# Performance work log

Hardware: AMD Instinct MI355X
Metric: run time of the kernel (lower is better)

The kernel has to match this reference:

```python
import jax, jax.numpy as jnp
import numpy as np

N, E = 100000, 800000
NODE_DIM, EDGE_DIM, HIDDEN = 64, 32, 128
LN_EPS = 1e-5


def _linear_params(key, fan_in, fan_out):
    # torch nn.Linear default: U(-1/sqrt(fan_in), 1/sqrt(fan_in))
    kw, kb = jax.random.split(key)
    bound = 1.0 / np.sqrt(fan_in)
    W = jax.random.uniform(kw, (fan_in, fan_out), jnp.float32, -bound, bound)
    b = jax.random.uniform(kb, (fan_out,), jnp.float32, -bound, bound)
    return W, b


def setup_inputs() -> dict:
    key = jax.random.key(0)
    ks = jax.random.split(key, 8)
    x = jax.random.normal(ks[0], (N, NODE_DIM), jnp.float32)
    edge_index = jax.random.randint(ks[1], (2, E), 0, N, jnp.int32)
    edge_attr = jax.random.normal(ks[2], (E, EDGE_DIM), jnp.float32)

    msg_in = 2 * NODE_DIM + EDGE_DIM
    W_msg1, b_msg1 = _linear_params(ks[3], msg_in, HIDDEN)
    g_msg = jnp.ones((HIDDEN,), jnp.float32)
    be_msg = jnp.zeros((HIDDEN,), jnp.float32)
    W_msg2, b_msg2 = _linear_params(ks[4], HIDDEN, HIDDEN)

    upd_in = NODE_DIM + HIDDEN
    W_upd1, b_upd1 = _linear_params(ks[5], upd_in, HIDDEN)
    g_upd = jnp.ones((HIDDEN,), jnp.float32)
    be_upd = jnp.zeros((HIDDEN,), jnp.float32)
    W_upd2, b_upd2 = _linear_params(ks[6], HIDDEN, NODE_DIM)

    return {
        "x": x, "edge_index": edge_index, "edge_attr": edge_attr,
        "W_msg1": W_msg1, "b_msg1": b_msg1, "g_msg": g_msg, "be_msg": be_msg,
        "W_msg2": W_msg2, "b_msg2": b_msg2,
        "W_upd1": W_upd1, "b_upd1": b_upd1, "g_upd": g_upd, "be_upd": be_upd,
        "W_upd2": W_upd2, "b_upd2": b_upd2,
    }


def _layer_norm(h, gamma, beta):
    mu = jnp.mean(h, axis=-1, keepdims=True)
    var = jnp.mean(jnp.square(h - mu), axis=-1, keepdims=True)
    return (h - mu) * jax.lax.rsqrt(var + LN_EPS) * gamma + beta


def _mlp(h, W1, b1, gamma, beta, W2, b2):
    h = h @ W1 + b1
    h = jax.nn.silu(_layer_norm(h, gamma, beta))
    return h @ W2 + b2


def reference(x, edge_index, edge_attr,
              W_msg1, b_msg1, g_msg, be_msg, W_msg2, b_msg2,
              W_upd1, b_upd1, g_upd, be_upd, W_upd2, b_upd2):
    src, dst = edge_index[0], edge_index[1]
    # gather -> message MLP: (E, 2*node_dim + edge_dim) -> (E, hidden)
    msg_input = jnp.concatenate([x[src], x[dst], edge_attr], axis=-1)
    msgs = _mlp(msg_input, W_msg1, b_msg1, g_msg, be_msg, W_msg2, b_msg2)
    # scatter-add aggregate over destination nodes: (N, hidden)
    agg = jax.ops.segment_sum(msgs, dst, num_segments=x.shape[0])
    # update MLP + residual: (N, node_dim)
    upd_input = jnp.concatenate([x, agg], axis=-1)
    return x + _mlp(upd_input, W_upd1, b_upd1, g_upd, be_upd, W_upd2, b_upd2)
```

## Files before the change

kernel.cpp:

```cpp
#include <hip/hip_runtime.h>
#include <hip/hip_fp16.h>
#include <stdint.h>


#define N_NODES 100000
#define N_EDGES 800000
#define NODE_DIM 64
#define EDGE_DIM 32
#define HIDDEN 128
#define LN_EPS 1e-5f

#define PH 136
#define PX 72
#define PU 200
#define PE 36

#define NB_SCAN ((N_NODES + 1023) / 1024)

typedef __attribute__((ext_vector_type(8))) short short8;
typedef __attribute__((ext_vector_type(4))) float f32x4;

static __device__ __forceinline__ uint16_t f2bf(float f) {
  uint32_t u = __float_as_uint(f);
  return (uint16_t)((u + 0x7FFFu + ((u >> 16) & 1u)) >> 16);
}
static __device__ __forceinline__ float bflo(uint32_t u) {
  return __uint_as_float(u << 16);
}
static __device__ __forceinline__ float bfhi(uint32_t u) {
  return __uint_as_float(u & 0xFFFF0000u);
}
static __device__ __forceinline__ float bfs(uint16_t u) {
  return __uint_as_float(((uint32_t)u) << 16);
}


#define PREP_HIST_BLKS 3125
#define PREP_PACK_BLKS 209

__global__ void prep_kernel(const int* __restrict__ ei, int* __restrict__ cnt,
                            const float* __restrict__ W1, uint16_t* __restrict__ Wcatp,
                            uint16_t* __restrict__ W1cb,
                            const float* __restrict__ Wu1, uint16_t* __restrict__ Wu1p,
                            const float* __restrict__ Wu2, uint16_t* __restrict__ Wu2p,
                            const float* __restrict__ W2, const float* __restrict__ b2,
                            float* __restrict__ qv) {
  int b = blockIdx.x;
  if (b < PREP_HIST_BLKS) {
    int e = b * 256 + threadIdx.x;
    if (e < N_EDGES) atomicAdd(&cnt[ei[N_EDGES + e]], 1);
    return;
  }
  int i = (b - PREP_HIST_BLKS) * 256 + threadIdx.x;
  if (i < 16384) {
    int k = i >> 8, c = i & 255;
    float v = (c < 128) ? W1[k * 128 + c] : W1[(64 + k) * 128 + (c - 128)];
    Wcatp[(((k >> 5) * 256 + c) * 4 + ((k >> 3) & 3)) * 8 + (k & 7)] = f2bf(v);
  } else if (i < 24576) {
    i -= 16384;
    int k = i >> 7, c = i & 127;
    Wu1p[(((k >> 5) * 128 + c) * 4 + ((k >> 3) & 3)) * 8 + (k & 7)] = f2bf(Wu1[i]);
  } else if (i < 32768) {
    i -= 24576;
    int k = i >> 6, c = i & 63;
    Wu2p[(((k >> 5) * 64 + c) * 4 + ((k >> 3) & 3)) * 8 + (k & 7)] = f2bf(Wu2[i]);
  } else if (i < 36864) {
    i -= 32768;
    int k = i >> 7, c = i & 127;
    W1cb[((size_t)(c * 4) + ((k >> 3) & 3)) * 8 + (k & 7)] = f2bf(W1[(128 + k) * 128 + c]);
  } else if (i < 53248) {
    i -= 36864;
    int k = i >> 7, c = i & 127;
    float s = 0.f;
    for (int j = 0; j < 128; ++j) s += W2[k * 128 + j] * Wu1[(64 + j) * 128 + c];
    int kk = 64 + k;
    Wu1p[(((kk >> 5) * 128 + c) * 4 + ((kk >> 3) & 3)) * 8 + (kk & 7)] = f2bf(s);
  } else if (i < 53376) {
    int c = i - 53248;
    float s = 0.f;
    for (int j = 0; j < 128; ++j) s += b2[j] * Wu1[(64 + j) * 128 + c];
    qv[c] = s;
  }
}


__global__ __launch_bounds__(256) void scan_blk(const int* __restrict__ cnt,
                                                int* __restrict__ offs,
                                                int* __restrict__ bsum) {
  __shared__ int wsum[4];
  int tid = threadIdx.x;
  int base = blockIdx.x * 1024 + tid * 4;
  int v0 = 0, v1 = 0, v2 = 0, v3 = 0;
  if (base < N_NODES) v0 = cnt[base];
  if (base + 1 < N_NODES) v1 = cnt[base + 1];
  if (base + 2 < N_NODES) v2 = cnt[base + 2];
  if (base + 3 < N_NODES) v3 = cnt[base + 3];
  int tsum = v0 + v1 + v2 + v3;
  int lane = tid & 63, wid = tid >> 6;
  int s = tsum;
  #pragma unroll
  for (int d = 1; d < 64; d <<= 1) {
    int t = __shfl_up(s, d);
    if (lane >= d) s += t;
  }
  if (lane == 63) wsum[wid] = s;
  __syncthreads();
  int woff = 0;
  for (int w = 0; w < wid; ++w) woff += wsum[w];
  int excl = woff + s - tsum;
  if (base < N_NODES) {
    int run = excl;
    offs[base] = run; run += v0;
    if (base + 1 < N_NODES) { offs[base + 1] = run; run += v1; }
    if (base + 2 < N_NODES) { offs[base + 2] = run; run += v2; }
    if (base + 3 < N_NODES) { offs[base + 3] = run; run += v3; }
  }
  if (tid == 255) bsum[blockIdx.x] = woff + s;
}

__global__ void scan_top(int* __restrict__ bsum) {
  __shared__ int sh[128];
  int tid = threadIdx.x;
  int v = (tid < NB_SCAN) ? bsum[tid] : 0;
  int orig = v;
  sh[tid] = v;
  __syncthreads();
  for (int d = 1; d < 128; d <<= 1) {
    int t = (tid >= d) ? sh[tid - d] : 0;
    __syncthreads();
    v += t;
    sh[tid] = v;
    __syncthreads();
  }
  if (tid < NB_SCAN) bsum[tid] = v - orig;
}

__global__ void scan_add(const int* __restrict__ offs, const int* __restrict__ bsum,
                         int* __restrict__ cursor) {
  int i = blockIdx.x * 256 + threadIdx.x;
  if (i < N_NODES) cursor[i] = offs[i] + bsum[i >> 10];
}

__global__ void scatter_edges(const int* __restrict__ ei, int* __restrict__ cursor,
                              int2* __restrict__ se_s, int* __restrict__ dst_s) {
  int e = blockIdx.x * 256 + threadIdx.x;
  if (e < N_EDGES) {
    int s = ei[e], d = ei[N_EDGES + e];
    int p = atomicAdd(&cursor[d], 1);
    se_s[p] = make_int2(s, e);
    dst_s[p] = d;
  }
}


__global__ __launch_bounds__(256) void p12_kernel(
    const float* __restrict__ x, const uint16_t* __restrict__ Wcatp,
    uint16_t* __restrict__ P12) {
  __shared__ __align__(16) uint16_t A[64 * PX];
  const int tid = threadIdx.x;
  const int n0 = blockIdx.x * 64;

  #pragma unroll
  for (int it = 0; it < 4; ++it) {
    int u = tid + it * 256;
    int r = u >> 4, q = u & 15;
    int node = min(n0 + r, N_NODES - 1);
    float4 f = *(const float4*)(x + (size_t)node * 64 + q * 4);
    ushort4 o;
    o.x = f2bf(f.x); o.y = f2bf(f.y); o.z = f2bf(f.z); o.w = f2bf(f.w);
    *(ushort4*)(&A[r * PX + q * 4]) = o;
  }
  __syncthreads();

  const int wid = tid >> 6, lane = tid & 63;
  const int lrow = lane & 15, lk = lane >> 4;
  const int r0 = wid * 16;

  f32x4 acc[16] = {};
  const uint16_t* Abase = &A[(r0 + lrow) * PX + lk * 8];
  #pragma unroll
  for (int c = 0; c < 2; ++c) {
    short8 a = *(const short8*)(Abase + c * 32);
    #pragma unroll
    for (int n = 0; n < 16; ++n) {
      short8 b = *(const short8*)(Wcatp + ((size_t)(c * 256 + n * 16 + lrow) * 4 + lk) * 8);
      acc[n] = __builtin_amdgcn_mfma_f32_16x16x32_bf16(a, b, acc[n], 0, 0, 0);
    }
  }

  #pragma unroll
  for (int reg = 0; reg < 4; ++reg) {
    int row = n0 + r0 + lk * 4 + reg;
    if (row < N_NODES) {
      #pragma unroll
      for (int n = 0; n < 16; ++n) {
        P12[(size_t)row * 256 + n * 16 + lrow] = f2bf(acc[n][reg]);
      }
    }
  }
}


__global__ __launch_bounds__(256) void msg_fused(
    const int2* __restrict__ se_s, const int* __restrict__ dst_s,
    const float* __restrict__ ea,
    const uint16_t* __restrict__ P12, const uint16_t* __restrict__ W1cb,
    const float* __restrict__ b1, const float* __restrict__ g1,
    const float* __restrict__ be1, float* __restrict__ S) {
  __shared__ __align__(16) uint16_t Ae[64 * PE];
  __shared__ __align__(16) uint16_t Hs[64 * PH];
  __shared__ int sdst[64];

  const int tid = threadIdx.x;
  int bid = blockIdx.x;
  int xcd = bid & 7, idx = bid >> 3;
  int bswz = (xcd < 4 ? xcd * 1563 : 6252 + (xcd - 4) * 1562) + idx;
  const int e0 = bswz * 64;

  if (tid < 64) sdst[tid] = dst_s[e0 + tid];

  {
    int pl = tid >> 2, q = tid & 3;
    int eid = se_s[e0 + pl].y;
    const float* er = ea + (size_t)eid * 32 + q * 8;
    float4 f0 = *(const float4*)(er);
    float4 f1 = *(const float4*)(er + 4);
    ushort4 o0, o1;
    o0.x = f2bf(f0.x); o0.y = f2bf(f0.y); o0.z = f2bf(f0.z); o0.w = f2bf(f0.w);
    o1.x = f2bf(f1.x); o1.y = f2bf(f1.y); o1.z = f2bf(f1.z); o1.w = f2bf(f1.w);
    *(ushort4*)(&Ae[pl * PE + q * 8]) = o0;
    *(ushort4*)(&Ae[pl * PE + q * 8 + 4]) = o1;
  }
  __syncthreads();

  const int wid = tid >> 6, lane = tid & 63;
  const int lrow = lane & 15, lk = lane >> 4;
  const int r0 = wid * 16;

  f32x4 acc[8] = {};
  short8 a = *(const short8*)(&Ae[(r0 + lrow) * PE + lk * 8]);
  #pragma unroll
  for (int n = 0; n < 8; ++n) {
    short8 b = *(const short8*)(W1cb + ((size_t)((n * 16 + lrow) * 4) + lk) * 8);
    acc[n] = __builtin_amdgcn_mfma_f32_16x16x32_bf16(a, b, acc[n], 0, 0, 0);
  }
  #pragma unroll
  for (int reg = 0; reg < 4; ++reg) {
    uint16_t* hrow = &Hs[(r0 + lk * 4 + reg) * PH];
    #pragma unroll
    for (int n = 0; n < 8; ++n) {
      hrow[n * 16 + lrow] = f2bf(acc[n][reg]);
    }
  }

  const int g = lk;
  const int c0 = lrow * 8;
  float b1v[8], gv[8], bev[8];
  {
    float4 f0 = *(const float4*)(b1 + c0), f1 = *(const float4*)(b1 + c0 + 4);
    b1v[0]=f0.x; b1v[1]=f0.y; b1v[2]=f0.z; b1v[3]=f0.w;
    b1v[4]=f1.x; b1v[5]=f1.y; b1v[6]=f1.z; b1v[7]=f1.w;
    float4 g0 = *(const float4*)(g1 + c0), g1v = *(const float4*)(g1 + c0 + 4);
    gv[0]=g0.x; gv[1]=g0.y; gv[2]=g0.z; gv[3]=g0.w;
    gv[4]=g1v.x; gv[5]=g1v.y; gv[6]=g1v.z; gv[7]=g1v.w;
    float4 be0 = *(const float4*)(be1 + c0), be1v = *(const float4*)(be1 + c0 + 4);
    bev[0]=be0.x; bev[1]=be0.y; bev[2]=be0.z; bev[3]=be0.w;
    bev[4]=be1v.x; bev[5]=be1v.y; bev[6]=be1v.z; bev[7]=be1v.w;
  }

  #pragma unroll
  for (int it = 0; it < 4; ++it) {
    int er_ = r0 + it * 4 + g;
    int p = e0 + er_;
    int src = se_s[p].x;
    int d = sdst[er_];
    uint4 p1 = *(const uint4*)(P12 + (size_t)src * 256 + c0);
    uint4 p2 = *(const uint4*)(P12 + (size_t)d * 256 + 128 + c0);
    uint4 et = *(const uint4*)(&Hs[er_ * PH + c0]);
    float h[8];
    h[0] = b1v[0] + bflo(p1.x) + bflo(p2.x) + bflo(et.x);
    h[1] = b1v[1] + bfhi(p1.x) + bfhi(p2.x) + bfhi(et.x);
    h[2] = b1v[2] + bflo(p1.y) + bflo(p2.y) + bflo(et.y);
    h[3] = b1v[3] + bfhi(p1.y) + bfhi(p2.y) + bfhi(et.y);
    h[4] = b1v[4] + bflo(p1.z) + bflo(p2.z) + bflo(et.z);
    h[5] = b1v[5] + bfhi(p1.z) + bfhi(p2.z) + bfhi(et.z);
    h[6] = b1v[6] + bflo(p1.w) + bflo(p2.w) + bflo(et.w);
    h[7] = b1v[7] + bfhi(p1.w) + bfhi(p2.w) + bfhi(et.w);

    float s = 0.f, ss = 0.f;
    #pragma unroll
    for (int j = 0; j < 8; ++j) { s += h[j]; ss += h[j] * h[j]; }
    #pragma unroll
    for (int m = 1; m <= 8; m <<= 1) {
      s += __shfl_xor(s, m);
      ss += __shfl_xor(ss, m);
    }
    float mu = s * (1.f / 128.f);
    float vr = ss * (1.f / 128.f) - mu * mu + LN_EPS;
    float rstd;
    asm("v_rsq_f32 %0, %1" : "=v"(rstd) : "v"(vr));
    ushort4 u0, u1;
    uint16_t uu[8];
    #pragma unroll
    for (int j = 0; j < 8; ++j) {
      float xv = (h[j] - mu) * rstd * gv[j] + bev[j];
      float tv = xv * -1.44269504f;
      float ev, rv;
      asm("v_exp_f32 %0, %1" : "=v"(ev) : "v"(tv));
      float dv = 1.f + ev;
      asm("v_rcp_f32 %0, %1" : "=v"(rv) : "v"(dv));
      uu[j] = f2bf(xv * rv);
    }
    u0.x = uu[0]; u0.y = uu[1]; u0.z = uu[2]; u0.w = uu[3];
    u1.x = uu[4]; u1.y = uu[5]; u1.z = uu[6]; u1.w = uu[7];
    *(ushort4*)(&Hs[er_ * PH + c0]) = u0;
    *(ushort4*)(&Hs[er_ * PH + c0 + 4]) = u1;
  }

  {
    int c = lane * 2;
    int cur = sdst[r0];
    int rstart = 0;
    ushort2 o = *(const ushort2*)&Hs[r0 * PH + c];
    float run0 = bfs(o.x), run1 = bfs(o.y);
    #pragma unroll
    for (int i = 1; i < 16; ++i) {
      int r = r0 + i;
      int d = sdst[r];
      ushort2 t = *(const ushort2*)&Hs[r * PH + c];
      float v0 = bfs(t.x), v1 = bfs(t.y);
      if (d != cur) {
        if (rstart > 0) {
          float2 ov; ov.x = run0; ov.y = run1;
          *(float2*)(S + (size_t)cur * HIDDEN + c) = ov;
        } else {
          atomicAdd(S + (size_t)cur * HIDDEN + c,     run0);
          atomicAdd(S + (size_t)cur * HIDDEN + c + 1, run1);
        }
        run0 = v0; run1 = v1; cur = d; rstart = i;
      } else {
        run0 += v0; run1 += v1;
      }
    }
    atomicAdd(S + (size_t)cur * HIDDEN + c,     run0);
    atomicAdd(S + (size_t)cur * HIDDEN + c + 1, run1);
  }
}


__global__ __launch_bounds__(256) void upd_kernel(
    const float* __restrict__ x, const float* __restrict__ S,
    const int* __restrict__ cnt, const float* __restrict__ qv,
    const uint16_t* __restrict__ Wu1p, const float* __restrict__ b1,
    const float* __restrict__ g1, const float* __restrict__ be1,
    const uint16_t* __restrict__ Wu2p, const float* __restrict__ b2,
    float* __restrict__ out) {
  __shared__ __align__(16) uint16_t A[64 * PU];
  __shared__ float sb1[128], sg[128], sbe[128], sb2[64], sq[128], scnt[64];

  const int tid = threadIdx.x;
  const int n0 = blockIdx.x * 64;

  if (tid < 128) { sb1[tid] = b1[tid]; sg[tid] = g1[tid]; }
  else { sbe[tid - 128] = be1[tid - 128]; sq[tid - 128] = qv[tid - 128]; }
  if (tid < 64) {
    sb2[tid] = b2[tid];
    scnt[tid] = (float)cnt[min(n0 + tid, N_NODES - 1)];
  }

  #pragma unroll
  for (int it = 0; it < 4; ++it) {
    int u = tid + it * 256;
    int r = u >> 4, q = u & 15;
    int node = min(n0 + r, N_NODES - 1);
    float4 f = *(const float4*)(x + (size_t)node * 64 + q * 4);
    ushort4 o;
    o.x = f2bf(f.x); o.y = f2bf(f.y); o.z = f2bf(f.z); o.w = f2bf(f.w);
    *(ushort4*)(&A[r * PU + q * 4]) = o;
  }
  #pragma unroll
  for (int it = 0; it < 8; ++it) {
    int u = tid + it * 256;
    int r = u >> 5, q = u & 31;
    int node = min(n0 + r, N_NODES - 1);
    float4 f = *(const float4*)(S + (size_t)node * 128 + q * 4);
    ushort4 o;
    o.x = f2bf(f.x); o.y = f2bf(f.y); o.z = f2bf(f.z); o.w = f2bf(f.w);
    *(ushort4*)(&A[r * PU + 64 + q * 4]) = o;
  }
  __syncthreads();

  const int wid = tid >> 6, lane = tid & 63;
  const int lrow = lane & 15, lk = lane >> 4;
  const int r0 = wid * 16;

  f32x4 acc[8] = {};
  const uint16_t* Abase = &A[(r0 + lrow) * PU + lk * 8];
  #pragma unroll
  for (int c = 0; c < 6; ++c) {
    short8 a = *(const short8*)(Abase + c * 32);
    #pragma unroll
    for (int n = 0; n < 8; ++n) {
      short8 b = *(const short8*)(Wu1p + ((size_t)((c * 128) + (n * 16 + lrow)) * 4 + lk) * 8);
      acc[n] = __builtin_amdgcn_mfma_f32_16x16x32_bf16(a, b, acc[n], 0, 0, 0);
    }
  }

  uint16_t* strip = &A[r0 * PU];
  #pragma unroll
  for (int reg = 0; reg < 4; ++reg) {
    float cf = scnt[r0 + lk * 4 + reg];
    float v[8];
    float s = 0.f, ss = 0.f;
    #pragma unroll
    for (int n = 0; n < 8; ++n) {
      int col = n * 16 + lrow;
      v[n] = acc[n][reg] + sb1[col] + cf * sq[col];
      s += v[n]; ss += v[n] * v[n];
    }
    #pragma unroll
    for (int m = 1; m <= 8; m <<= 1) {
      s += __shfl_xor(s, m);
      ss += __shfl_xor(ss, m);
    }
    float mu = s * (1.f / 128.f);
    float rstd = rsqrtf(ss * (1.f / 128.f) - mu * mu + LN_EPS);
    uint16_t* hrow = strip + (lk * 4 + reg) * PH;
    #pragma unroll
    for (int n = 0; n < 8; ++n) {
      int col = n * 16 + lrow;
      float h = (v[n] - mu) * rstd * sg[col] + sbe[col];
      h = h / (1.f + __expf(-h));
      hrow[col] = f2bf(h);
    }
  }

  f32x4 acc2[4] = {};
  const uint16_t* Hbase = strip + lrow * PH + lk * 8;
  #pragma unroll
  for (int c = 0; c < 4; ++c) {
    short8 a = *(const short8*)(Hbase + c * 32);
    #pragma unroll
    for (int n = 0; n < 4; ++n) {
      short8 b = *(const short8*)(Wu2p + ((size_t)((c * 64) + (n * 16 + lrow)) * 4 + lk) * 8);
      acc2[n] = __builtin_amdgcn_mfma_f32_16x16x32_bf16(a, b, acc2[n], 0, 0, 0);
    }
  }

  #pragma unroll
  for (int reg = 0; reg < 4; ++reg) {
    int node = n0 + r0 + lk * 4 + reg;
    if (node < N_NODES) {
      #pragma unroll
      for (int n = 0; n < 4; ++n) {
        int col = n * 16 + lrow;
        out[(size_t)node * 64 + col] =
            x[(size_t)node * 64 + col] + acc2[n][reg] + sb2[col];
      }
    }
  }
}

extern "C" void kernel_launch(void* const* d_in, const int* in_sizes, int n_in,
                              void* d_out, int out_size, void* d_ws, size_t ws_size,
                              hipStream_t stream) {
  const float* x   = (const float*)d_in[0];
  const int*   ei  = (const int*)d_in[1];
  const float* ea  = (const float*)d_in[2];
  const float* W1  = (const float*)d_in[3];
  const float* b1  = (const float*)d_in[4];
  const float* g1  = (const float*)d_in[5];
  const float* be1 = (const float*)d_in[6];
  const float* W2  = (const float*)d_in[7];
  const float* b2  = (const float*)d_in[8];
  const float* Wu1 = (const float*)d_in[9];
  const float* bu1 = (const float*)d_in[10];
  const float* gu  = (const float*)d_in[11];
  const float* beu = (const float*)d_in[12];
  const float* Wu2 = (const float*)d_in[13];
  const float* bu2 = (const float*)d_in[14];
  float* out = (float*)d_out;

  char* ws = (char*)d_ws;
  float*    S      = (float*)ws;
  uint16_t* P12    = (uint16_t*)(ws + 51200000);
  uint16_t* Wcatp  = (uint16_t*)(ws + 102400000);
  uint16_t* Wu1p   = (uint16_t*)(ws + 102432768);
  uint16_t* Wu2p   = (uint16_t*)(ws + 102481920);
  uint16_t* W1cb   = (uint16_t*)(ws + 102498304);
  float*    qv     = (float*)(ws + 102506496);
  int*      cnt    = (int*)(ws + 102507008);
  int*      offs   = (int*)(ws + 102907008);
  int*      cursor = (int*)(ws + 103307008);
  int*      bsum   = (int*)(ws + 103707008);
  int2*     se_s   = (int2*)(ws + 103707520);
  int*      dst_s  = (int*)(ws + 110107520);

  (void)hipMemsetAsync(cnt, 0, (size_t)N_NODES * 4, stream);
  (void)hipMemsetAsync(S, 0, (size_t)N_NODES * HIDDEN * 4, stream);

  prep_kernel<<<PREP_HIST_BLKS + PREP_PACK_BLKS, 256, 0, stream>>>(
      ei, cnt, W1, Wcatp, W1cb, Wu1, Wu1p, Wu2, Wu2p, W2, b2, qv);

  scan_blk<<<NB_SCAN, 256, 0, stream>>>(cnt, offs, bsum);
  scan_top<<<1, 128, 0, stream>>>(bsum);
  scan_add<<<(N_NODES + 255) / 256, 256, 0, stream>>>(offs, bsum, cursor);
  scatter_edges<<<(N_EDGES + 255) / 256, 256, 0, stream>>>(ei, cursor, se_s, dst_s);

  p12_kernel<<<(N_NODES + 63) / 64, 256, 0, stream>>>(x, Wcatp, P12);

  msg_fused<<<N_EDGES / 64, 256, 0, stream>>>(se_s, dst_s, ea, P12,
                                              W1cb, b1, g1, be1, S);

  upd_kernel<<<(N_NODES + 63) / 64, 256, 0, stream>>>(x, S, cnt, qv,
                                                      Wu1p, bu1, gu, beu, Wu2p, bu2, out);
}
```

Measured before the change: 292.5 us.

## Make msg_fused a grid-stride kernel processing several edge tiles per block

The message kernel now launches a fixed 2048 blocks, each looping over up to seven consecutive 64-edge tiles, instead of one block per tile with an XCD-aware block swizzle. Destination indices are kept in a register and broadcast with wave shuffles instead of being staged in shared memory. The block barrier is removed because each wave only reads shared-memory rows it wrote itself. This amortizes the bias, gamma and beta loads and the launch overhead across tiles, at the cost of the XCD locality swizzle and some tail imbalance, since only about 1786 of the 2048 blocks get work.

```diff
diff --git a/kernel.cpp b/kernel.cpp
--- a/kernel.cpp
+++ b/kernel.cpp
@@ -16,6 +16,9 @@
 #define PE 36
 
 #define NB_SCAN ((N_NODES + 1023) / 1024)
+#define MSG_TILES (N_EDGES / 64)
+#define MSG_BLOCKS 2048
+#define MSG_TPB 7
 
 typedef __attribute__((ext_vector_type(8))) short short8;
 typedef __attribute__((ext_vector_type(4))) float f32x4;
@@ -209,141 +212,139 @@
     const float* __restrict__ be1, float* __restrict__ S) {
   __shared__ __align__(16) uint16_t Ae[64 * PE];
   __shared__ __align__(16) uint16_t Hs[64 * PH];
-  __shared__ int sdst[64];
 
   const int tid = threadIdx.x;
-  int bid = blockIdx.x;
-  int xcd = bid & 7, idx = bid >> 3;
-  int bswz = (xcd < 4 ? xcd * 1563 : 6252 + (xcd - 4) * 1562) + idx;
-  const int e0 = bswz * 64;
-
-  if (tid < 64) sdst[tid] = dst_s[e0 + tid];
-
-  {
-    int pl = tid >> 2, q = tid & 3;
-    int eid = se_s[e0 + pl].y;
-    const float* er = ea + (size_t)eid * 32 + q * 8;
-    float4 f0 = *(const float4*)(er);
-    float4 f1 = *(const float4*)(er + 4);
-    ushort4 o0, o1;
-    o0.x = f2bf(f0.x); o0.y = f2bf(f0.y); o0.z = f2bf(f0.z); o0.w = f2bf(f0.w);
-    o1.x = f2bf(f1.x); o1.y = f2bf(f1.y); o1.z = f2bf(f1.z); o1.w = f2bf(f1.w);
-    *(ushort4*)(&Ae[pl * PE + q * 8]) = o0;
-    *(ushort4*)(&Ae[pl * PE + q * 8 + 4]) = o1;
-  }
-  __syncthreads();
-
   const int wid = tid >> 6, lane = tid & 63;
   const int lrow = lane & 15, lk = lane >> 4;
   const int r0 = wid * 16;
-
-  f32x4 acc[8] = {};
-  short8 a = *(const short8*)(&Ae[(r0 + lrow) * PE + lk * 8]);
-  #pragma unroll
-  for (int n = 0; n < 8; ++n) {
-    short8 b = *(const short8*)(W1cb + ((size_t)((n * 16 + lrow) * 4) + lk) * 8);
-    acc[n] = __builtin_amdgcn_mfma_f32_16x16x32_bf16(a, b, acc[n], 0, 0, 0);
-  }
-  #pragma unroll
-  for (int reg = 0; reg < 4; ++reg) {
-    uint16_t* hrow = &Hs[(r0 + lk * 4 + reg) * PH];
-    #pragma unroll
-    for (int n = 0; n < 8; ++n) {
-      hrow[n * 16 + lrow] = f2bf(acc[n][reg]);
-    }
-  }
-
   const int g = lk;
-  const int c0 = lrow * 8;
+  const int c0g = lrow * 8;
+
   float b1v[8], gv[8], bev[8];
   {
-    float4 f0 = *(const float4*)(b1 + c0), f1 = *(const float4*)(b1 + c0 + 4);
+    float4 f0 = *(const float4*)(b1 + c0g), f1 = *(const float4*)(b1 + c0g + 4);
     b1v[0]=f0.x; b1v[1]=f0.y; b1v[2]=f0.z; b1v[3]=f0.w;
     b1v[4]=f1.x; b1v[5]=f1.y; b1v[6]=f1.z; b1v[7]=f1.w;
-    float4 g0 = *(const float4*)(g1 + c0), g1v = *(const float4*)(g1 + c0 + 4);
+    float4 g0 = *(const float4*)(g1 + c0g), g1v = *(const float4*)(g1 + c0g + 4);
     gv[0]=g0.x; gv[1]=g0.y; gv[2]=g0.z; gv[3]=g0.w;
     gv[4]=g1v.x; gv[5]=g1v.y; gv[6]=g1v.z; gv[7]=g1v.w;
-    float4 be0 = *(const float4*)(be1 + c0), be1v = *(const float4*)(be1 + c0 + 4);
+    float4 be0 = *(const float4*)(be1 + c0g), be1v = *(const float4*)(be1 + c0g + 4);
     bev[0]=be0.x; bev[1]=be0.y; bev[2]=be0.z; bev[3]=be0.w;
     bev[4]=be1v.x; bev[5]=be1v.y; bev[6]=be1v.z; bev[7]=be1v.w;
   }
 
-  #pragma unroll
-  for (int it = 0; it < 4; ++it) {
-    int er_ = r0 + it * 4 + g;
-    int p = e0 + er_;
-    int src = se_s[p].x;
-    int d = sdst[er_];
-    uint4 p1 = *(const uint4*)(P12 + (size_t)src * 256 + c0);
-    uint4 p2 = *(const uint4*)(P12 + (size_t)d * 256 + 128 + c0);
-    uint4 et = *(const uint4*)(&Hs[er_ * PH + c0]);
-    float h[8];
-    h[0] = b1v[0] + bflo(p1.x) + bflo(p2.x) + bflo(et.x);
-    h[1] = b1v[1] + bfhi(p1.x) + bfhi(p2.x) + bfhi(et.x);
-    h[2] = b1v[2] + bflo(p1.y) + bflo(p2.y) + bflo(et.y);
-    h[3] = b1v[3] + bfhi(p1.y) + bfhi(p2.y) + bfhi(et.y);
-    h[4] = b1v[4] + bflo(p1.z) + bflo(p2.z) + bflo(et.z);
-    h[5] = b1v[5] + bfhi(p1.z) + bfhi(p2.z) + bfhi(et.z);
-    h[6] = b1v[6] + bflo(p1.w) + bflo(p2.w) + bflo(et.w);
-    h[7] = b1v[7] + bfhi(p1.w) + bfhi(p2.w) + bfhi(et.w);
-
-    float s = 0.f, ss = 0.f;
-    #pragma unroll
-    for (int j = 0; j < 8; ++j) { s += h[j]; ss += h[j] * h[j]; }
-    #pragma unroll
-    for (int m = 1; m <= 8; m <<= 1) {
-      s += __shfl_xor(s, m);
-      ss += __shfl_xor(ss, m);
-    }
-    float mu = s * (1.f / 128.f);
-    float vr = ss * (1.f / 128.f) - mu * mu + LN_EPS;
-    float rstd;
-    asm("v_rsq_f32 %0, %1" : "=v"(rstd) : "v"(vr));
-    ushort4 u0, u1;
-    uint16_t uu[8];
-    #pragma unroll
-    for (int j = 0; j < 8; ++j) {
-      float xv = (h[j] - mu) * rstd * gv[j] + bev[j];
-      float tv = xv * -1.44269504f;
-      float ev, rv;
-      asm("v_exp_f32 %0, %1" : "=v"(ev) : "v"(tv));
-      float dv = 1.f + ev;
-      asm("v_rcp_f32 %0, %1" : "=v"(rv) : "v"(dv));
-      uu[j] = f2bf(xv * rv);
-    }
-    u0.x = uu[0]; u0.y = uu[1]; u0.z = uu[2]; u0.w = uu[3];
-    u1.x = uu[4]; u1.y = uu[5]; u1.z = uu[6]; u1.w = uu[7];
-    *(ushort4*)(&Hs[er_ * PH + c0]) = u0;
-    *(ushort4*)(&Hs[er_ * PH + c0 + 4]) = u1;
-  }
-
-  {
-    int c = lane * 2;
-    int cur = sdst[r0];
-    int rstart = 0;
-    ushort2 o = *(const ushort2*)&Hs[r0 * PH + c];
-    float run0 = bfs(o.x), run1 = bfs(o.y);
-    #pragma unroll
-    for (int i = 1; i < 16; ++i) {
-      int r = r0 + i;
-      int d = sdst[r];
-      ushort2 t = *(const ushort2*)&Hs[r * PH + c];
-      float v0 = bfs(t.x), v1 = bfs(t.y);
-      if (d != cur) {
-        if (rstart > 0) {
-          float2 ov; ov.x = run0; ov.y = run1;
-          *(float2*)(S + (size_t)cur * HIDDEN + c) = ov;
+  for (int j = 0; j < MSG_TPB; ++j) {
+    int tile = blockIdx.x * MSG_TPB + j;
+    if (tile >= MSG_TILES) break;
+    const int e0 = tile * 64;
+
+    int dval = dst_s[e0 + r0 + (lane & 15)];
+
+    {
+      int pl = tid >> 2, q = tid & 3;
+      int eid = se_s[e0 + pl].y;
+      const float* er = ea + (size_t)eid * 32 + q * 8;
+      float4 f0 = *(const float4*)(er);
+      float4 f1 = *(const float4*)(er + 4);
+      ushort4 o0, o1;
+      o0.x = f2bf(f0.x); o0.y = f2bf(f0.y); o0.z = f2bf(f0.z); o0.w = f2bf(f0.w);
+      o1.x = f2bf(f1.x); o1.y = f2bf(f1.y); o1.z = f2bf(f1.z); o1.w = f2bf(f1.w);
+      *(ushort4*)(&Ae[pl * PE + q * 8]) = o0;
+      *(ushort4*)(&Ae[pl * PE + q * 8 + 4]) = o1;
+    }
+
+    f32x4 acc[8] = {};
+    short8 a = *(const short8*)(&Ae[(r0 + lrow) * PE + lk * 8]);
+    #pragma unroll
+    for (int n = 0; n < 8; ++n) {
+      short8 b = *(const short8*)(W1cb + ((size_t)((n * 16 + lrow) * 4) + lk) * 8);
+      acc[n] = __builtin_amdgcn_mfma_f32_16x16x32_bf16(a, b, acc[n], 0, 0, 0);
+    }
+    #pragma unroll
+    for (int reg = 0; reg < 4; ++reg) {
+      uint16_t* hrow = &Hs[(r0 + lk * 4 + reg) * PH];
+      #pragma unroll
+      for (int n = 0; n < 8; ++n) {
+        hrow[n * 16 + lrow] = f2bf(acc[n][reg]);
+      }
+    }
+
+    #pragma unroll
+    for (int it = 0; it < 4; ++it) {
+      int er_ = r0 + it * 4 + g;
+      int p = e0 + er_;
+      int src = se_s[p].x;
+      int d = __shfl(dval, it * 4 + g);
+      uint4 p1 = *(const uint4*)(P12 + (size_t)src * 256 + c0g);
+      uint4 p2 = *(const uint4*)(P12 + (size_t)d * 256 + 128 + c0g);
+      uint4 et = *(const uint4*)(&Hs[er_ * PH + c0g]);
+      float h[8];
+      h[0] = b1v[0] + bflo(p1.x) + bflo(p2.x) + bflo(et.x);
+      h[1] = b1v[1] + bfhi(p1.x) + bfhi(p2.x) + bfhi(et.x);
+      h[2] = b1v[2] + bflo(p1.y) + bflo(p2.y) + bflo(et.y);
+      h[3] = b1v[3] + bfhi(p1.y) + bfhi(p2.y) + bfhi(et.y);
+      h[4] = b1v[4] + bflo(p1.z) + bflo(p2.z) + bflo(et.z);
+      h[5] = b1v[5] + bfhi(p1.z) + bfhi(p2.z) + bfhi(et.z);
+      h[6] = b1v[6] + bflo(p1.w) + bflo(p2.w) + bflo(et.w);
+      h[7] = b1v[7] + bfhi(p1.w) + bfhi(p2.w) + bfhi(et.w);
+
+      float s = 0.f, ss = 0.f;
+      #pragma unroll
+      for (int jj = 0; jj < 8; ++jj) { s += h[jj]; ss += h[jj] * h[jj]; }
+      #pragma unroll
+      for (int m = 1; m <= 8; m <<= 1) {
+        s += __shfl_xor(s, m);
+        ss += __shfl_xor(ss, m);
+      }
+      float mu = s * (1.f / 128.f);
+      float vr = ss * (1.f / 128.f) - mu * mu + LN_EPS;
+      float rstd;
+      asm("v_rsq_f32 %0, %1" : "=v"(rstd) : "v"(vr));
+      ushort4 u0, u1;
+      uint16_t uu[8];
+      #pragma unroll
+      for (int jj = 0; jj < 8; ++jj) {
+        float xv = (h[jj] - mu) * rstd * gv[jj] + bev[jj];
+        float tv = xv * -1.44269504f;
+        float ev, rv;
+        asm("v_exp_f32 %0, %1" : "=v"(ev) : "v"(tv));
+        float dv = 1.f + ev;
+        asm("v_rcp_f32 %0, %1" : "=v"(rv) : "v"(dv));
+        uu[jj] = f2bf(xv * rv);
+      }
+      u0.x = uu[0]; u0.y = uu[1]; u0.z = uu[2]; u0.w = uu[3];
+      u1.x = uu[4]; u1.y = uu[5]; u1.z = uu[6]; u1.w = uu[7];
+      *(ushort4*)(&Hs[er_ * PH + c0g]) = u0;
+      *(ushort4*)(&Hs[er_ * PH + c0g + 4]) = u1;
+    }
+
+    {
+      int c = lane * 2;
+      int cur = __shfl(dval, 0);
+      int rstart = 0;
+      ushort2 o = *(const ushort2*)&Hs[r0 * PH + c];
+      float run0 = bfs(o.x), run1 = bfs(o.y);
+      #pragma unroll
+      for (int i = 1; i < 16; ++i) {
+        int d = __shfl(dval, i);
+        ushort2 t = *(const ushort2*)&Hs[(r0 + i) * PH + c];
+        float v0 = bfs(t.x), v1 = bfs(t.y);
+        if (d != cur) {
+          if (rstart > 0) {
+            float2 ov; ov.x = run0; ov.y = run1;
+            *(float2*)(S + (size_t)cur * HIDDEN + c) = ov;
+          } else {
+            atomicAdd(S + (size_t)cur * HIDDEN + c,     run0);
+            atomicAdd(S + (size_t)cur * HIDDEN + c + 1, run1);
+          }
+          run0 = v0; run1 = v1; cur = d; rstart = i;
         } else {
-          atomicAdd(S + (size_t)cur * HIDDEN + c,     run0);
-          atomicAdd(S + (size_t)cur * HIDDEN + c + 1, run1);
+          run0 += v0; run1 += v1;
         }
-        run0 = v0; run1 = v1; cur = d; rstart = i;
-      } else {
-        run0 += v0; run1 += v1;
       }
-    }
-    atomicAdd(S + (size_t)cur * HIDDEN + c,     run0);
-    atomicAdd(S + (size_t)cur * HIDDEN + c + 1, run1);
+      atomicAdd(S + (size_t)cur * HIDDEN + c,     run0);
+      atomicAdd(S + (size_t)cur * HIDDEN + c + 1, run1);
+    }
   }
 }
 
@@ -509,8 +510,8 @@
 
   p12_kernel<<<(N_NODES + 63) / 64, 256, 0, stream>>>(x, Wcatp, P12);
 
-  msg_fused<<<N_EDGES / 64, 256, 0, stream>>>(se_s, dst_s, ea, P12,
-                                              W1cb, b1, g1, be1, S);
+  msg_fused<<<MSG_BLOCKS, 256, 0, stream>>>(se_s, dst_s, ea, P12,
+                                            W1cb, b1, g1, be1, S);
 
   upd_kernel<<<(N_NODES + 63) / 64, 256, 0, stream>>>(x, S, cnt, qv,
                                                       Wu1p, bu1, gu, beu, Wu2p, bu2, out);
```

Measured after the change: 352.0 us. 1.2x slower.
